# Kernel tuning notes

Hardware: AMD Instinct MI355X
Metric: run time of the kernel (lower is better)

Reference implementation:

```python
import jax, jax.numpy as jnp
import numpy as np

TOKENS_PER_SCALE = [1, 4, 16, 64, 256]  # CLS + 2x2,4x4,8x8,16x16 patch scales = 341
TOTAL = sum(TOKENS_PER_SCALE)
NUM_HEADS = 12


def build_scale_causal_mask():
    # 0 where allowed, -inf where blocked. CLS row (scale 0) attends everywhere;
    # tokens in scale i may attend to scales j <= i (and always to CLS).
    cum = np.cumsum([0] + TOKENS_PER_SCALE)
    m = np.zeros((TOTAL, TOTAL), dtype=np.float32)
    for i in range(1, len(TOKENS_PER_SCALE)):
        for j in range(len(TOKENS_PER_SCALE)):
            if j > i:
                m[cum[i]:cum[i + 1], cum[j]:cum[j + 1]] = -np.inf
    return jnp.asarray(m)


def setup_inputs() -> dict:
    key = jax.random.key(0)
    k1, k2, k3, k4, k5 = jax.random.split(key, 5)
    B, N, D = 64, TOTAL, 768
    x = jax.random.normal(k1, (B, N, D), dtype=jnp.float32)
    qkv_w = jax.random.normal(k2, (3 * D, D), dtype=jnp.float32) * 0.02
    qkv_b = jax.random.normal(k3, (3 * D,), dtype=jnp.float32) * 0.02
    proj_w = jax.random.normal(k4, (D, D), dtype=jnp.float32) * 0.02
    proj_b = jax.random.normal(k5, (D,), dtype=jnp.float32) * 0.02
    return {"x": x, "qkv_w": qkv_w, "qkv_b": qkv_b, "proj_w": proj_w, "proj_b": proj_b}


def reference(x, qkv_w, qkv_b, proj_w, proj_b):
    B, N, D = x.shape
    H = NUM_HEADS
    hd = D // H
    scale = hd ** -0.5
    mask = build_scale_causal_mask()  # [N, N]

    qkv = jnp.einsum('bnd,ed->bne', x, qkv_w) + qkv_b  # [B, N, 3D]
    qkv = qkv.reshape(B, N, 3, H, hd)
    q = jnp.transpose(qkv[:, :, 0], (0, 2, 1, 3))  # [B, H, N, hd]
    k = jnp.transpose(qkv[:, :, 1], (0, 2, 1, 3))
    v = jnp.transpose(qkv[:, :, 2], (0, 2, 1, 3))

    attn = jnp.einsum('bhqd,bhkd->bhqk', q, k) * scale + mask  # [B, H, N, N]
    attn = jax.nn.softmax(attn, axis=-1)
    out = jnp.einsum('bhqk,bhkd->bhqd', attn, v)  # [B, H, N, hd]
    out = jnp.transpose(out, (0, 2, 1, 3)).reshape(B, N, D)
    out = jnp.einsum('bnd,ed->bne', out, proj_w) + proj_b
    return out
```

## Files before the change

### kernel.cpp

```cpp
#include <hip/hip_runtime.h>
#include <hip/hip_bf16.h>

typedef float  f32x4  __attribute__((ext_vector_type(4)));
typedef __bf16 bf16x4 __attribute__((ext_vector_type(4)));
typedef __bf16 bf16x8 __attribute__((ext_vector_type(8)));

#define B_SZ  64
#define NTOK  341
#define DM    768
#define NH    12
#define HD    64
#define MTOT  (B_SZ*NTOK)
#define MP    21888
#define EQKV  2304

#define EXP2F(x) __builtin_amdgcn_exp2f(x)

__device__ __forceinline__ void gload_lds16(const __bf16* g, void* l) {
    __builtin_amdgcn_global_load_lds(
        (const __attribute__((address_space(1))) void*)g,
        (__attribute__((address_space(3))) void*)l, 16, 0, 0);
}

__global__ void cvt_kernel(const float* __restrict__ in, __bf16* __restrict__ out, int n4) {
    int i = blockIdx.x * blockDim.x + threadIdx.x;
    const int stride = gridDim.x * blockDim.x;
    for (; i < n4; i += stride) {
        const float4 f = ((const float4*)in)[i];
        bf16x4 v;
        v[0] = (__bf16)f.x; v[1] = (__bf16)f.y; v[2] = (__bf16)f.z; v[3] = (__bf16)f.w;
        ((bf16x4*)out)[i] = v;
    }
}

template <int EPI, int EN, int NT>
__global__ __launch_bounds__(256) void gemm128(
    const __bf16* __restrict__ A, const __bf16* __restrict__ Bw,
    const float* __restrict__ bias,
    __bf16* __restrict__ obf, float* __restrict__ of32)
{
    __shared__ __bf16 As[2][128 * 64];
    __shared__ __bf16 Bs[2][128 * 64];

    const int tid  = threadIdx.x;
    const int lane = tid & 63;
    const int w    = tid >> 6;
    const int wm   = w >> 1, wn = w & 1;
    const int qi   = lane & 15;
    const int g    = lane >> 4;

    const int nwg = gridDim.x;
    const int bid = blockIdx.x;
    const int qq = nwg >> 3, rr = nwg & 7;
    const int xcd = bid & 7, idx = bid >> 3;
    const int wg = (xcd < rr ? xcd * (qq + 1) : rr * (qq + 1) + (xcd - rr) * qq) + idx;
    const int mtile = wg / NT;
    const int ntile = wg % NT;
    const long a_row0 = (long)mtile * 128;
    const long n0     = (long)ntile * 128;

    const int slot = lane & 7;
    const __bf16* aP[4];
    const __bf16* bP[4];
#pragma unroll
    for (int it = 0; it < 4; ++it) {
        const int lrow = it * 32 + w * 8 + (lane >> 3);
        const int scol = (slot ^ (lrow & 7)) * 8;
        aP[it] = A + (a_row0 + lrow) * DM + scol;
        const int gcol = (lrow & 64) | ((lrow & 15) << 2) | ((lrow >> 4) & 3);
        bP[it] = Bw + (n0 + gcol) * DM + scol;
    }

    const f32x4 fzero = {0.f, 0.f, 0.f, 0.f};
    f32x4 acc[4][4];
#pragma unroll
    for (int i = 0; i < 4; ++i)
#pragma unroll
        for (int j = 0; j < 4; ++j) acc[i][j] = fzero;

#define STAGE(P, K0) do { \
    _Pragma("unroll") for (int it = 0; it < 4; ++it) { \
        gload_lds16(aP[it] + (K0), (char*)(&As[P][0]) + it * 4096 + w * 1024); \
        gload_lds16(bP[it] + (K0), (char*)(&Bs[P][0]) + it * 4096 + w * 1024); \
    } } while (0)

    STAGE(0, 0);
    __syncthreads();

    int cur = 0;
    for (int k0 = 0; k0 < DM; k0 += 64) {
        if (k0 + 64 < DM) STAGE(cur ^ 1, k0 + 64);

        const __bf16* pA = &As[cur][0];
        const __bf16* pB = &Bs[cur][0];
        bf16x8 af[4][2], bfr[4][2];
#pragma unroll
        for (int i = 0; i < 4; ++i) {
            const int fr = wm * 64 + i * 16 + qi;
#pragma unroll
            for (int ks = 0; ks < 2; ++ks)
                af[i][ks] = *(const bf16x8*)(pA + fr * 64 + (((ks << 2) + g) ^ (fr & 7)) * 8);
        }
#pragma unroll
        for (int j = 0; j < 4; ++j) {
            const int frb = wn * 64 + j * 16 + qi;
#pragma unroll
            for (int ks = 0; ks < 2; ++ks)
                bfr[j][ks] = *(const bf16x8*)(pB + frb * 64 + (((ks << 2) + g) ^ (frb & 7)) * 8);
        }
#pragma unroll
        for (int ks = 0; ks < 2; ++ks)
#pragma unroll
            for (int j = 0; j < 4; ++j)
#pragma unroll
                for (int i = 0; i < 4; ++i)
                    acc[i][j] = __builtin_amdgcn_mfma_f32_16x16x32_bf16(
                        af[i][ks], bfr[j][ks], acc[i][j], 0, 0, 0);

        __syncthreads();
        cur ^= 1;
    }
#undef STAGE

    const long ge0 = n0 + wn * 64 + qi * 4;
    const float4 b4 = *(const float4*)(bias + ge0);
    const float mul = (EPI == 0 && (n0 + wn * 64) < DM) ? 0.125f * 1.44269504f : 1.f;
#pragma unroll
    for (int i = 0; i < 4; ++i) {
#pragma unroll
        for (int r = 0; r < 4; ++r) {
            const long m = a_row0 + wm * 64 + i * 16 + g * 4 + r;
            if (m < MTOT) {
                if (EPI == 0) {
                    bf16x4 pv;
                    pv[0] = (__bf16)((acc[i][0][r] + b4.x) * mul);
                    pv[1] = (__bf16)((acc[i][1][r] + b4.y) * mul);
                    pv[2] = (__bf16)((acc[i][2][r] + b4.z) * mul);
                    pv[3] = (__bf16)((acc[i][3][r] + b4.w) * mul);
                    *(bf16x4*)(obf + m * EN + ge0) = pv;
                } else {
                    float4 o;
                    o.x = acc[i][0][r] + b4.x;
                    o.y = acc[i][1][r] + b4.y;
                    o.z = acc[i][2][r] + b4.z;
                    o.w = acc[i][3][r] + b4.w;
                    *(float4*)(of32 + m * EN + ge0) = o;
                }
            }
        }
    }
}

__global__ __launch_bounds__(512) void attn_kernel(
    const __bf16* __restrict__ qkv, __bf16* __restrict__ ao)
{
    const int h = blockIdx.x;
    const int b = blockIdx.y;
    const long rowb = (long)b * NTOK;

    __shared__ char vL[64 * 768];

    const int tid  = threadIdx.x;
    const int lane = tid & 63;
    const int w    = tid >> 6;

#pragma unroll
    for (int it = 0; it < 6; ++it) {
        const int c = it * 512 + tid;
        if (c < 2816) {
            const int n  = c >> 3;
            const int dc = (c & 7) << 3;
            bf16x8 e;
            if (n < NTOK) e = *(const bf16x8*)(qkv + (rowb + n) * EQKV + 1536 + h * HD + dc);
            else { e[0]=e[1]=e[2]=e[3]=e[4]=e[5]=e[6]=e[7] = (__bf16)0.f; }
            const int s   = ((n >> 5) << 2) | ((n >> 2) & 3);
            const int off = (((n >> 4) & 1) << 3) | ((n & 3) << 1);
            const int x   = c & 7;
#pragma unroll
            for (int i = 0; i < 8; ++i) {
                const int sp = s ^ i ^ x;
                *(__bf16*)(vL + (dc + i) * 768 + sp * 16 + off) = e[i];
            }
        }
    }
    __syncthreads();

    const int g  = lane >> 4;
    const int qi = lane & 15;

    bf16x8 qf0[3], qf1[3];
    int   qg[3], limit[3];
#pragma unroll
    for (int s = 0; s < 3; ++s) {
        const int gi = w + 8 * s;
        const int q  = gi * 16 + qi;
        qg[s] = q;
        const int qrow = (q > NTOK - 1) ? (NTOK - 1) : q;
        const __bf16* qsrc = qkv + (rowb + qrow) * EQKV + h * HD + g * 8;
        qf0[s] = *(const bf16x8*)(qsrc);
        qf1[s] = *(const bf16x8*)(qsrc + 32);
        limit[s] = (q == 0) ? NTOK : (q < 5 ? 5 : (q < 21 ? 21 : (q < 85 ? 85 : NTOK)));
    }

    const f32x4 fzero = {0.f, 0.f, 0.f, 0.f};
    f32x4 oacc[3][4];
    float sum[3] = {0.f, 0.f, 0.f};
#pragma unroll
    for (int s = 0; s < 3; ++s)
#pragma unroll
        for (int db = 0; db < 4; ++db) oacc[s][db] = fzero;

    const __bf16* kbase = qkv + rowb * EQKV + DM + h * HD + g * 8;
    const int xd = (qi & 7) ^ ((qi >> 3) & 7);

    for (int j = 0; j < 11; ++j) {
        const int kr0 = 32 * j + qi;
        int kr1 = kr0 + 16; if (kr1 > NTOK - 1) kr1 = NTOK - 1;
        const __bf16* k0p = kbase + (long)kr0 * EQKV;
        const __bf16* k1p = kbase + (long)kr1 * EQKV;
        const bf16x8 k00 = *(const bf16x8*)(k0p);
        const bf16x8 k01 = *(const bf16x8*)(k0p + 32);
        const bf16x8 k10 = *(const bf16x8*)(k1p);
        const bf16x8 k11 = *(const bf16x8*)(k1p + 32);

        bf16x8 pf[3];
#pragma unroll
        for (int s = 0; s < 3; ++s) {
            f32x4 s0 = __builtin_amdgcn_mfma_f32_16x16x32_bf16(k00, qf0[s], fzero, 0, 0, 0);
            s0 = __builtin_amdgcn_mfma_f32_16x16x32_bf16(k01, qf1[s], s0, 0, 0, 0);
            f32x4 s1 = __builtin_amdgcn_mfma_f32_16x16x32_bf16(k10, qf0[s], fzero, 0, 0, 0);
            s1 = __builtin_amdgcn_mfma_f32_16x16x32_bf16(k11, qf1[s], s1, 0, 0, 0);
#pragma unroll
            for (int r = 0; r < 4; ++r) {
                const int k0i = 32 * j + g * 4 + r;
                const float p0 = (k0i < limit[s]) ? EXP2F(s0[r]) : 0.f;
                sum[s] += p0; pf[s][r] = (__bf16)p0;
                const int k1i = k0i + 16;
                const float p1 = (k1i < limit[s]) ? EXP2F(s1[r]) : 0.f;
                sum[s] += p1; pf[s][4 + r] = (__bf16)p1;
            }
        }

#pragma unroll
        for (int db = 0; db < 4; ++db) {
            const int d  = db * 16 + qi;
            const int sp = (4 * j + g) ^ xd ^ ((2 * db) & 7);
            const bf16x8 vf = *(const bf16x8*)(vL + d * 768 + sp * 16);
#pragma unroll
            for (int s = 0; s < 3; ++s)
                oacc[s][db] = __builtin_amdgcn_mfma_f32_16x16x32_bf16(
                    vf, pf[s], oacc[s][db], 0, 0, 0);
        }
    }

#pragma unroll
    for (int s = 0; s < 3; ++s) {
        float t = sum[s];
        t += __shfl_xor(t, 16);
        t += __shfl_xor(t, 32);
        const float rinv = 1.f / t;
        if (qg[s] < NTOK) {
            const long orow = (rowb + qg[s]) * DM + h * HD;
#pragma unroll
            for (int db = 0; db < 4; ++db) {
                bf16x4 pv;
#pragma unroll
                for (int r = 0; r < 4; ++r) pv[r] = (__bf16)(oacc[s][db][r] * rinv);
                *(bf16x4*)(ao + orow + db * 16 + g * 4) = pv;
            }
        }
    }
}

extern "C" void kernel_launch(void* const* d_in, const int* in_sizes, int n_in,
                              void* d_out, int out_size, void* d_ws, size_t ws_size,
                              hipStream_t stream) {
    const float* x      = (const float*)d_in[0];
    const float* qkv_w  = (const float*)d_in[1];
    const float* qkv_b  = (const float*)d_in[2];
    const float* proj_w = (const float*)d_in[3];
    const float* proj_b = (const float*)d_in[4];
    float* out = (float*)d_out;

    char* ws = (char*)d_ws;
    constexpr size_t XB_BYTES  = (size_t)MP * DM * 2;
    constexpr size_t WQ_OFF    = XB_BYTES;
    constexpr size_t WP_OFF    = WQ_OFF + (size_t)EQKV * DM * 2;
    constexpr size_t QKV_OFF   = WP_OFF + (size_t)DM * DM * 2;

    __bf16* xb  = (__bf16*)(ws);
    __bf16* wq  = (__bf16*)(ws + WQ_OFF);
    __bf16* wp  = (__bf16*)(ws + WP_OFF);
    __bf16* qkv = (__bf16*)(ws + QKV_OFF);

    cvt_kernel<<<2048, 256, 0, stream>>>(x,      xb, MTOT * DM / 4);
    cvt_kernel<<<1728, 256, 0, stream>>>(qkv_w,  wq, EQKV * DM / 4);
    cvt_kernel<<<576,  256, 0, stream>>>(proj_w, wp, DM * DM / 4);

    gemm128<0, EQKV, 18><<<171 * 18, 256, 0, stream>>>(xb, wq, qkv_b, qkv, nullptr);
    attn_kernel<<<dim3(NH, B_SZ), 512, 0, stream>>>(qkv, xb);
    gemm128<1, DM, 6><<<171 * 6, 256, 0, stream>>>(xb, wp, proj_b, nullptr, out);
}
```

Before: 239.8 us.

## Merge fp32-to-bf16 conversions into one launch and prefetch K in attention

Combines the three fp32-to-bf16 conversion launches into a single grid-stride kernel that walks x, qkv_w and proj_w in turn. This removes two kernel launches and their tail gaps. In the attention kernel, Q fragments and the first K tile are now loaded before the V staging into LDS, so those global loads overlap it. The K loop double-buffers in registers, prefetching the next tile's K rows while the current tile runs its MFMAs. This raises register pressure and adds branching in the conversion loop.

```diff
diff --git a/kernel.cpp b/kernel.cpp
--- a/kernel.cpp
+++ b/kernel.cpp
@@ -22,14 +22,23 @@
         (__attribute__((address_space(3))) void*)l, 16, 0, 0);
 }
 
-__global__ void cvt_kernel(const float* __restrict__ in, __bf16* __restrict__ out, int n4) {
+__global__ void cvt3_kernel(const float* __restrict__ x,  __bf16* __restrict__ xb,
+                            const float* __restrict__ wqf, __bf16* __restrict__ wq,
+                            const float* __restrict__ wpf, __bf16* __restrict__ wp) {
+    constexpr int N1 = MTOT * DM / 4;
+    constexpr int N2 = EQKV * DM / 4;
+    constexpr int N3 = DM * DM / 4;
     int i = blockIdx.x * blockDim.x + threadIdx.x;
     const int stride = gridDim.x * blockDim.x;
-    for (; i < n4; i += stride) {
-        const float4 f = ((const float4*)in)[i];
+    for (; i < N1 + N2 + N3; i += stride) {
+        const float* src; __bf16* dst; int k;
+        if (i < N1)           { src = x;   dst = xb; k = i; }
+        else if (i < N1 + N2) { src = wqf; dst = wq; k = i - N1; }
+        else                  { src = wpf; dst = wp; k = i - N1 - N2; }
+        const float4 f = ((const float4*)src)[k];
         bf16x4 v;
         v[0] = (__bf16)f.x; v[1] = (__bf16)f.y; v[2] = (__bf16)f.z; v[3] = (__bf16)f.w;
-        ((bf16x4*)out)[i] = v;
+        ((bf16x4*)dst)[k] = v;
     }
 }
 
@@ -163,6 +172,38 @@
     const int tid  = threadIdx.x;
     const int lane = tid & 63;
     const int w    = tid >> 6;
+    const int g    = lane >> 4;
+    const int qi   = lane & 15;
+
+    const __bf16* kbase = qkv + rowb * EQKV + DM + h * HD + g * 8;
+
+    bf16x8 qf0[3], qf1[3];
+    int qg[3], limit[3];
+#pragma unroll
+    for (int s = 0; s < 3; ++s) {
+        const int gi = w + 8 * s;
+        const int q  = gi * 16 + qi;
+        qg[s] = q;
+        const int qrow = (q > NTOK - 1) ? (NTOK - 1) : q;
+        const __bf16* qsrc = qkv + (rowb + qrow) * EQKV + h * HD + g * 8;
+        qf0[s] = *(const bf16x8*)(qsrc);
+        qf1[s] = *(const bf16x8*)(qsrc + 32);
+        limit[s] = (q == 0) ? NTOK : (q < 5 ? 5 : (q < 21 ? 21 : (q < 85 ? 85 : NTOK)));
+    }
+
+#define LOADK(BUF, J) do { \
+    const int kr0_ = 32 * (J) + qi; \
+    int kr1_ = kr0_ + 16; if (kr1_ > NTOK - 1) kr1_ = NTOK - 1; \
+    const __bf16* k0p_ = kbase + (long)kr0_ * EQKV; \
+    const __bf16* k1p_ = kbase + (long)kr1_ * EQKV; \
+    BUF[0] = *(const bf16x8*)(k0p_); \
+    BUF[1] = *(const bf16x8*)(k0p_ + 32); \
+    BUF[2] = *(const bf16x8*)(k1p_); \
+    BUF[3] = *(const bf16x8*)(k1p_ + 32); \
+} while (0)
+
+    bf16x8 kr[2][4];
+    LOADK(kr[0], 0);
 
 #pragma unroll
     for (int it = 0; it < 6; ++it) {
@@ -185,23 +226,6 @@
     }
     __syncthreads();
 
-    const int g  = lane >> 4;
-    const int qi = lane & 15;
-
-    bf16x8 qf0[3], qf1[3];
-    int   qg[3], limit[3];
-#pragma unroll
-    for (int s = 0; s < 3; ++s) {
-        const int gi = w + 8 * s;
-        const int q  = gi * 16 + qi;
-        qg[s] = q;
-        const int qrow = (q > NTOK - 1) ? (NTOK - 1) : q;
-        const __bf16* qsrc = qkv + (rowb + qrow) * EQKV + h * HD + g * 8;
-        qf0[s] = *(const bf16x8*)(qsrc);
-        qf1[s] = *(const bf16x8*)(qsrc + 32);
-        limit[s] = (q == 0) ? NTOK : (q < 5 ? 5 : (q < 21 ? 21 : (q < 85 ? 85 : NTOK)));
-    }
-
     const f32x4 fzero = {0.f, 0.f, 0.f, 0.f};
     f32x4 oacc[3][4];
     float sum[3] = {0.f, 0.f, 0.f};
@@ -210,26 +234,19 @@
 #pragma unroll
         for (int db = 0; db < 4; ++db) oacc[s][db] = fzero;
 
-    const __bf16* kbase = qkv + rowb * EQKV + DM + h * HD + g * 8;
     const int xd = (qi & 7) ^ ((qi >> 3) & 7);
 
+#pragma unroll 2
     for (int j = 0; j < 11; ++j) {
-        const int kr0 = 32 * j + qi;
-        int kr1 = kr0 + 16; if (kr1 > NTOK - 1) kr1 = NTOK - 1;
-        const __bf16* k0p = kbase + (long)kr0 * EQKV;
-        const __bf16* k1p = kbase + (long)kr1 * EQKV;
-        const bf16x8 k00 = *(const bf16x8*)(k0p);
-        const bf16x8 k01 = *(const bf16x8*)(k0p + 32);
-        const bf16x8 k10 = *(const bf16x8*)(k1p);
-        const bf16x8 k11 = *(const bf16x8*)(k1p + 32);
+        if (j + 1 < 11) LOADK(kr[(j + 1) & 1], j + 1);
 
         bf16x8 pf[3];
 #pragma unroll
         for (int s = 0; s < 3; ++s) {
-            f32x4 s0 = __builtin_amdgcn_mfma_f32_16x16x32_bf16(k00, qf0[s], fzero, 0, 0, 0);
-            s0 = __builtin_amdgcn_mfma_f32_16x16x32_bf16(k01, qf1[s], s0, 0, 0, 0);
-            f32x4 s1 = __builtin_amdgcn_mfma_f32_16x16x32_bf16(k10, qf0[s], fzero, 0, 0, 0);
-            s1 = __builtin_amdgcn_mfma_f32_16x16x32_bf16(k11, qf1[s], s1, 0, 0, 0);
+            f32x4 s0 = __builtin_amdgcn_mfma_f32_16x16x32_bf16(kr[j & 1][0], qf0[s], fzero, 0, 0, 0);
+            s0 = __builtin_amdgcn_mfma_f32_16x16x32_bf16(kr[j & 1][1], qf1[s], s0, 0, 0, 0);
+            f32x4 s1 = __builtin_amdgcn_mfma_f32_16x16x32_bf16(kr[j & 1][2], qf0[s], fzero, 0, 0, 0);
+            s1 = __builtin_amdgcn_mfma_f32_16x16x32_bf16(kr[j & 1][3], qf1[s], s1, 0, 0, 0);
 #pragma unroll
             for (int r = 0; r < 4; ++r) {
                 const int k0i = 32 * j + g * 4 + r;
@@ -252,6 +269,7 @@
                     vf, pf[s], oacc[s][db], 0, 0, 0);
         }
     }
+#undef LOADK
 
 #pragma unroll
     for (int s = 0; s < 3; ++s) {
@@ -293,9 +311,7 @@
     __bf16* wp  = (__bf16*)(ws + WP_OFF);
     __bf16* qkv = (__bf16*)(ws + QKV_OFF);
 
-    cvt_kernel<<<2048, 256, 0, stream>>>(x,      xb, MTOT * DM / 4);
-    cvt_kernel<<<1728, 256, 0, stream>>>(qkv_w,  wq, EQKV * DM / 4);
-    cvt_kernel<<<576,  256, 0, stream>>>(proj_w, wp, DM * DM / 4);
+    cvt3_kernel<<<2048, 256, 0, stream>>>(x, xb, qkv_w, wq, proj_w, wp);
 
     gemm128<0, EQKV, 18><<<171 * 18, 256, 0, stream>>>(xb, wq, qkv_b, qkv, nullptr);
     attn_kernel<<<dim3(NH, B_SZ), 512, 0, stream>>>(qkv, xb);
```

New measurement: 224.8 us. 6.2% less time.
